# Kernel tuning notes

Hardware: AMD Instinct MI355X
Metric: run time of the kernel (lower is better)

## Reference

```python
import jax, jax.numpy as jnp
import numpy as np

N = 50000      # n_nodes
E = 300000     # n_edges
R = 32         # n_relations
D = 256        # embedding_dim
H = 128        # bilstm_hidden_size (2H == D so gate dims line up, as the source requires)
I = 64         # input_dim (time-series feature dim)
B = 4096       # batch
S = 50         # seq_len
HOPS = 2       # context_hops


def setup_inputs() -> dict:
    key = jax.random.key(0)
    ks = jax.random.split(key, 20)
    sc = 0.02
    inp = {
        "ts": jax.random.normal(ks[0], (B, S, I), jnp.float32),
        "node_emb": jax.random.normal(ks[1], (N, D), jnp.float32) * sc,
        "rel_w": jax.random.normal(ks[2], (R, D), jnp.float32) * sc + 1.0,
        "gate_W": jax.random.normal(ks[3], (D, 2 * D), jnp.float32) * sc,
        "gate_b": jnp.zeros((D,), jnp.float32),
        "risk_W1": jax.random.normal(ks[4], (D, D), jnp.float32) * sc,
        "risk_b1": jnp.zeros((D,), jnp.float32),
        "risk_W2": jax.random.normal(ks[5], (D, D), jnp.float32) * sc,
        "risk_b2": jnp.zeros((D,), jnp.float32),
        # BiLSTM encoder params (torch gate order i,f,g,o), fwd + bwd directions
        "Wih_f": jax.random.normal(ks[6], (4 * H, I), jnp.float32) * sc,
        "Whh_f": jax.random.normal(ks[7], (4 * H, H), jnp.float32) * sc,
        "b_f": jnp.zeros((4 * H,), jnp.float32),
        "Wih_b": jax.random.normal(ks[8], (4 * H, I), jnp.float32) * sc,
        "Whh_b": jax.random.normal(ks[9], (4 * H, H), jnp.float32) * sc,
        "b_b": jnp.zeros((4 * H,), jnp.float32),
        "edge_index": jax.random.randint(ks[10], (2, E), 0, N, jnp.int32),
        "edge_type": jax.random.randint(ks[11], (E,), 0, R, jnp.int32),
        "node_indexes": jax.random.randint(ks[12], (B,), 0, N, jnp.int32),
    }
    return inp


def _lstm_dir(x, Wih, Whh, b, reverse):
    # x: [B, S, I] -> outputs [B, S, H]
    def step(carry, xt):
        h, c = carry
        g = xt @ Wih.T + h @ Whh.T + b          # [B, 4H]
        i, f, gg, o = jnp.split(g, 4, axis=-1)
        c = jax.nn.sigmoid(f) * c + jax.nn.sigmoid(i) * jnp.tanh(gg)
        h = jax.nn.sigmoid(o) * jnp.tanh(c)
        return (h, c), h
    h0 = jnp.zeros((x.shape[0], Whh.shape[1]), x.dtype)
    xs = jnp.swapaxes(x, 0, 1)                   # [S, B, I]
    _, hs = jax.lax.scan(step, (h0, h0), xs, reverse=reverse)
    return jnp.swapaxes(hs, 0, 1)                # [B, S, H]


def _gcn(emb, head, tail, edge_type, rel_w, n_hops):
    # relation-weighted multi-hop message passing: gather -> relation scale -> scatter-mean
    deg = jax.ops.segment_sum(jnp.ones((head.shape[0],), emb.dtype), head, num_segments=N)
    deg = jnp.clip(deg, 1.0)[:, None]
    out = emb
    acc = emb
    for _ in range(n_hops):
        msg = out[tail] * rel_w[edge_type]                      # [E, D]
        out = jax.ops.segment_sum(msg, head, num_segments=N) / deg
        acc = acc + out
    return acc / (n_hops + 1.0)


def reference(ts, node_emb, rel_w, gate_W, gate_b, risk_W1, risk_b1, risk_W2,
              risk_b2, Wih_f, Whh_f, b_f, Wih_b, Whh_b, b_b,
              edge_index, edge_type, node_indexes):
    head, tail = edge_index[0], edge_index[1]
    all_emb = _gcn(node_emb, head, tail, edge_type, rel_w, HOPS)
    struct = all_emb[node_indexes]                              # [B, D]
    # BiLSTM encoder, temporal embedding = mean over time of [B,S,2H]
    hf = _lstm_dir(ts, Wih_f, Whh_f, b_f, reverse=False)
    hb = _lstm_dir(ts, Wih_b, Whh_b, b_b, reverse=True)
    temporal = jnp.concatenate([hf, hb], axis=-1).mean(axis=1)  # [B, 2H] == [B, D]
    cat = jnp.concatenate([struct, temporal], axis=-1)          # [B, 2D]
    gate = jax.nn.sigmoid(cat @ gate_W.T + gate_b)              # [B, D]
    merged = gate * struct + (1.0 - gate) * temporal
    risk = jnp.tanh(merged @ risk_W1.T + risk_b1) @ risk_W2.T + risk_b2
    return jax.nn.sigmoid(risk.sum(axis=-1))                    # [B]
```

## Files before the change

kernel.cpp:

```cpp
#include <hip/hip_runtime.h>

#define N_NODES 50000
#define N_EDGES 300000
#define DIM 256
#define HID 128
#define INP 64
#define BATCH 4096
#define SEQ 50
#define SCAN_BLOCKS 196

typedef float f32x2 __attribute__((ext_vector_type(2)));
typedef float f32x4 __attribute__((ext_vector_type(4)));
typedef __bf16 bf16x2 __attribute__((ext_vector_type(2)));
typedef __bf16 bf16x8 __attribute__((ext_vector_type(8)));

__device__ __forceinline__ float sigmoidf_(float x) {
    return __builtin_amdgcn_rcpf(1.0f + __expf(-x));
}
__device__ __forceinline__ float tanhf_(float x) {
    return 1.0f - 2.0f * __builtin_amdgcn_rcpf(1.0f + __expf(2.0f * x));
}

__device__ __forceinline__ void barrier_lds_only() {
    asm volatile("s_waitcnt lgkmcnt(0)" ::: "memory");
    __builtin_amdgcn_s_barrier();
}

__global__ void k_prep(const float* __restrict__ Wih_f, const float* __restrict__ Whh_f,
                       const float* __restrict__ Wih_b, const float* __restrict__ Whh_b,
                       const float* __restrict__ gate_W, const float* __restrict__ risk_W1,
                       const float* __restrict__ risk_W2, const float* __restrict__ risk_b2,
                       __bf16* __restrict__ w2frag, __bf16* __restrict__ gwp,
                       __bf16* __restrict__ w1p, float* __restrict__ w2s,
                       int* __restrict__ deg, int* __restrict__ flagi) {
    __shared__ float red[256];
    int bid = blockIdx.x, tid = threadIdx.x;
    if (bid < 768) {
        int idx = bid * 256 + tid;
        int dir = idx / 98304;
        int rem = idx % 98304;
        int frag = rem >> 9;
        int within = rem & 511;
        int lane = within >> 3, j = within & 7;
        int kc = frag % 6;
        int wg = frag / 6;
        int g = wg & 3, w = wg >> 2;
        int n = g * 128 + w * 16 + (lane & 15);
        int k = kc * 32 + (lane >> 4) * 8 + j;
        const float* Wih = dir ? Wih_b : Wih_f;
        const float* Whh = dir ? Whh_b : Whh_f;
        float v = (k < 64) ? Wih[n * 64 + k] : Whh[n * 128 + (k - 64)];
        w2frag[idx] = (__bf16)v;
    } else if (bid < 1280) {
        int idx = (bid - 768) * 256 + tid;
        int frag = idx >> 9, within = idx & 511;
        int lane = within >> 3, j = within & 7;
        int kc = frag % 16, T = frag / 16;
        int n = T * 16 + (lane & 15);
        int k = kc * 32 + (lane >> 4) * 8 + j;
        gwp[idx] = (__bf16)gate_W[(size_t)n * 512 + k];
    } else if (bid < 1536) {
        int idx = (bid - 1280) * 256 + tid;
        int frag = idx >> 9, within = idx & 511;
        int lane = within >> 3, j = within & 7;
        int kc = frag % 8, T = frag / 8;
        int n = T * 16 + (lane & 15);
        int k = kc * 32 + (lane >> 4) * 8 + j;
        w1p[idx] = (__bf16)risk_W1[(size_t)n * 256 + k];
    } else if (bid == 1536) {
        int k = tid;
        float s = 0.0f;
        for (int n = 0; n < 256; n++) s += risk_W2[(size_t)n * 256 + k];
        w2s[k] = s;
        red[k] = risk_b2[k];
        __syncthreads();
        for (int st = 128; st > 0; st >>= 1) {
            if (k < st) red[k] += red[k + st];
            __syncthreads();
        }
        if (k == 0) w2s[256] = red[0];
    } else if (bid < 1733) {
        int i = (bid - 1537) * 256 + tid;
        if (i < N_NODES) deg[i] = 0;
    } else {
        int i = (bid - 1733) * 256 + tid;
        flagi[i] = 0;
    }
}


__global__ void k_hist(const int* __restrict__ head, int* __restrict__ deg) {
    int e = blockIdx.x * 256 + threadIdx.x;
    if (e < N_EDGES) atomicAdd(&deg[head[e]], 1);
}

__global__ void k_bsum(const int* __restrict__ deg, int* __restrict__ bsum) {
    __shared__ int red[256];
    int n = blockIdx.x * 256 + threadIdx.x;
    red[threadIdx.x] = (n < N_NODES) ? deg[n] : 0;
    __syncthreads();
    for (int st = 128; st > 0; st >>= 1) {
        if (threadIdx.x < st) red[threadIdx.x] += red[threadIdx.x + st];
        __syncthreads();
    }
    if (threadIdx.x == 0) bsum[blockIdx.x] = red[0];
}

__global__ void k_scanb(const int* __restrict__ bsum, int* __restrict__ boff) {
    __shared__ int s[256];
    int i = threadIdx.x;
    int v = (i < SCAN_BLOCKS) ? bsum[i] : 0;
    s[i] = v;
    __syncthreads();
    for (int st = 1; st < 256; st <<= 1) {
        int add = (i >= st) ? s[i - st] : 0;
        __syncthreads();
        s[i] += add;
        __syncthreads();
    }
    boff[i] = s[i] - v;
}

__global__ void k_scan2(const int* __restrict__ deg, const int* __restrict__ boff,
                        int* __restrict__ offsets, int* __restrict__ cursor) {
    __shared__ int s[256];
    int i = threadIdx.x;
    int n = blockIdx.x * 256 + i;
    int v = (n < N_NODES) ? deg[n] : 0;
    s[i] = v;
    __syncthreads();
    for (int st = 1; st < 256; st <<= 1) {
        int add = (i >= st) ? s[i - st] : 0;
        __syncthreads();
        s[i] += add;
        __syncthreads();
    }
    if (n < N_NODES) {
        int off = boff[blockIdx.x] + s[i] - v;
        offsets[n] = off;
        cursor[n] = off;
    }
    if (n == 0) offsets[N_NODES] = N_EDGES;
}

__global__ void k_place(const int* __restrict__ head, const int* __restrict__ tail,
                        const int* __restrict__ etype, int* __restrict__ cursor,
                        int* __restrict__ sorted) {
    int e = blockIdx.x * 256 + threadIdx.x;
    if (e >= N_EDGES) return;
    int h = head[e];
    int pos = atomicAdd(&cursor[h], 1);
    sorted[pos] = tail[e] | (etype[e] << 16);
}

__global__ void k_flag(const int* __restrict__ nidx, const int* __restrict__ offsets,
                       const int* __restrict__ sorted, char* __restrict__ flag) {
    int b = blockIdx.x * 256 + threadIdx.x;
    if (b >= BATCH) return;
    int n = nidx[b];
    flag[n] = 1;
    int s = offsets[n], e = offsets[n + 1];
    for (int j = s; j < e; j++) flag[sorted[j] & 0xFFFF] = 1;
}

__global__ void k_gather(const int* __restrict__ offsets, const int* __restrict__ sorted,
                         const float* __restrict__ relw, const float* __restrict__ src,
                         const char* __restrict__ flag, float* __restrict__ dst) {
    int tid = threadIdx.x;
    int w = tid >> 6, lane = tid & 63;
    int n = blockIdx.x * 4 + w;
    if (n >= N_NODES) return;
    if (!flag[n]) return;
    int s = offsets[n], e = offsets[n + 1];
    f32x4 acc0 = (f32x4){0.f, 0.f, 0.f, 0.f};
    f32x4 acc1 = (f32x4){0.f, 0.f, 0.f, 0.f};
    f32x4 acc2 = (f32x4){0.f, 0.f, 0.f, 0.f};
    f32x4 acc3 = (f32x4){0.f, 0.f, 0.f, 0.f};
    int j = s;
    for (; j + 4 <= e; j += 4) {
        int p0 = sorted[j], p1 = sorted[j + 1], p2 = sorted[j + 2], p3 = sorted[j + 3];
        f32x4 v0 = *(const f32x4*)(src + (size_t)(p0 & 0xFFFF) * DIM + lane * 4);
        f32x4 v1 = *(const f32x4*)(src + (size_t)(p1 & 0xFFFF) * DIM + lane * 4);
        f32x4 v2 = *(const f32x4*)(src + (size_t)(p2 & 0xFFFF) * DIM + lane * 4);
        f32x4 v3 = *(const f32x4*)(src + (size_t)(p3 & 0xFFFF) * DIM + lane * 4);
        acc0 += v0 * *(const f32x4*)(relw + (p0 >> 16) * DIM + lane * 4);
        acc1 += v1 * *(const f32x4*)(relw + (p1 >> 16) * DIM + lane * 4);
        acc2 += v2 * *(const f32x4*)(relw + (p2 >> 16) * DIM + lane * 4);
        acc3 += v3 * *(const f32x4*)(relw + (p3 >> 16) * DIM + lane * 4);
    }
    for (; j < e; j++) {
        int p0 = sorted[j];
        f32x4 v0 = *(const f32x4*)(src + (size_t)(p0 & 0xFFFF) * DIM + lane * 4);
        acc0 += v0 * *(const f32x4*)(relw + (p0 >> 16) * DIM + lane * 4);
    }
    acc0 = (acc0 + acc1) + (acc2 + acc3);
    float inv = 1.0f / fmaxf((float)(e - s), 1.0f);
    *(f32x4*)(dst + (size_t)n * DIM + lane * 4) = acc0 * inv;
}

__global__ void k_gather2(const int* __restrict__ nidx, const int* __restrict__ offsets,
                          const int* __restrict__ sorted, const float* __restrict__ relw,
                          const float* __restrict__ out1, const float* __restrict__ emb,
                          float* __restrict__ structb) {
    int tid = threadIdx.x;
    int w = tid >> 6, lane = tid & 63;
    int b = blockIdx.x * 4 + w;
    int n = nidx[b];
    int s = offsets[n], e = offsets[n + 1];
    f32x4 acc0 = (f32x4){0.f, 0.f, 0.f, 0.f};
    f32x4 acc1 = (f32x4){0.f, 0.f, 0.f, 0.f};
    f32x4 acc2 = (f32x4){0.f, 0.f, 0.f, 0.f};
    f32x4 acc3 = (f32x4){0.f, 0.f, 0.f, 0.f};
    int j = s;
    for (; j + 4 <= e; j += 4) {
        int p0 = sorted[j], p1 = sorted[j + 1], p2 = sorted[j + 2], p3 = sorted[j + 3];
        f32x4 v0 = *(const f32x4*)(out1 + (size_t)(p0 & 0xFFFF) * DIM + lane * 4);
        f32x4 v1 = *(const f32x4*)(out1 + (size_t)(p1 & 0xFFFF) * DIM + lane * 4);
        f32x4 v2 = *(const f32x4*)(out1 + (size_t)(p2 & 0xFFFF) * DIM + lane * 4);
        f32x4 v3 = *(const f32x4*)(out1 + (size_t)(p3 & 0xFFFF) * DIM + lane * 4);
        acc0 += v0 * *(const f32x4*)(relw + (p0 >> 16) * DIM + lane * 4);
        acc1 += v1 * *(const f32x4*)(relw + (p1 >> 16) * DIM + lane * 4);
        acc2 += v2 * *(const f32x4*)(relw + (p2 >> 16) * DIM + lane * 4);
        acc3 += v3 * *(const f32x4*)(relw + (p3 >> 16) * DIM + lane * 4);
    }
    for (; j < e; j++) {
        int p0 = sorted[j];
        f32x4 v0 = *(const f32x4*)(out1 + (size_t)(p0 & 0xFFFF) * DIM + lane * 4);
        acc0 += v0 * *(const f32x4*)(relw + (p0 >> 16) * DIM + lane * 4);
    }
    acc0 = (acc0 + acc1) + (acc2 + acc3);
    float inv = 1.0f / fmaxf((float)(e - s), 1.0f);
    f32x4 o2 = acc0 * inv;
    f32x4 e0 = *(const f32x4*)(emb + (size_t)n * DIM + lane * 4);
    f32x4 o1 = *(const f32x4*)(out1 + (size_t)n * DIM + lane * 4);
    *(f32x4*)(structb + (size_t)b * DIM + lane * 4) = (e0 + o1 + o2) * (1.0f / 3.0f);
}

__launch_bounds__(512)
__global__ void k_lstm(const float* __restrict__ ts, const __bf16* __restrict__ w2frag,
                       const float* __restrict__ b_f, const float* __restrict__ b_b,
                       float* __restrict__ temporal) {
    int dir = blockIdx.y;
    int btile = blockIdx.x;
    int tid = threadIdx.x;
    int w = tid >> 6;
    int lane = tid & 63;
    int col = lane & 15, quad = lane >> 4;

    __shared__ __align__(16) __bf16 SA[2 * 16 * 200];
    __shared__ __align__(16) __bf16 SB[2 * 16 * 200];

    for (int i = tid; i < 2048; i += 512) {
        int m = i >> 7, k = i & 127;
        SA[m * 200 + 64 + k] = (__bf16)0.0f;
        SB[m * 200 + 64 + k] = (__bf16)0.0f;
    }

    const float* bias = dir ? b_b : b_f;
    float bv[4];
#pragma unroll
    for (int g = 0; g < 4; g++) bv[g] = bias[g * 128 + w * 16 + col];

    const __bf16* wbase = w2frag + (size_t)dir * 98304 + (size_t)w * 12288;
    bf16x8 wreg[24];
#pragma unroll
    for (int f = 0; f < 24; f++) {
        wreg[f] = *(const bf16x8*)(wbase + (f << 9) + lane * 8);
    }

    int sm = tid >> 5, sc = (tid & 31) * 2;
    const float* xbA = ts + ((size_t)(btile * 32 + sm) * SEQ) * INP + sc;
    const float* xbB = ts + ((size_t)(btile * 32 + 16 + sm) * SEQ) * INP + sc;
    int t0i = dir ? (SEQ - 1) : 0;
    int t1i = dir ? (SEQ - 2) : 1;
    {
        f32x2 xa = *(const f32x2*)(xbA + (size_t)t0i * INP);
        f32x2 xb = *(const f32x2*)(xbB + (size_t)t0i * INP);
        bf16x2 va; va[0] = (__bf16)xa.x; va[1] = (__bf16)xa.y;
        bf16x2 vb; vb[0] = (__bf16)xb.x; vb[1] = (__bf16)xb.y;
        *(bf16x2*)&SA[sm * 200 + sc] = va;
        *(bf16x2*)&SB[sm * 200 + sc] = vb;
    }
    f32x2 xpreA = *(const f32x2*)(xbA + (size_t)t1i * INP);
    f32x2 xpreB = *(const f32x2*)(xbB + (size_t)t1i * INP);

    f32x4 cA = (f32x4){0.f, 0.f, 0.f, 0.f}, hsA = cA;
    f32x4 cB = cA, hsB = cA;
    f32x4 accA[4], accB[4];
    int hwr = quad * 4 * 200 + 64 + w * 16 + col;
    int ard = col * 200 + quad * 8;
    barrier_lds_only();

#pragma unroll
    for (int g = 0; g < 4; g++) accA[g] = (f32x4){bv[g], bv[g], bv[g], bv[g]};
#pragma unroll
    for (int kc = 0; kc < 6; kc++) {
        bf16x8 a0 = *(const bf16x8*)&SA[ard + kc * 32];
#pragma unroll
        for (int g = 0; g < 4; g++)
            accA[g] = __builtin_amdgcn_mfma_f32_16x16x32_bf16(a0, wreg[g * 6 + kc], accA[g], 0, 0, 0);
    }

    for (int t = 0; t < SEQ; t++) {
        int cb = (t & 1) * 3200;
        int nb = ((t + 1) & 1) * 3200;

        f32x2 xnA;
        bool ldA = (t + 2 < SEQ);
        if (ldA) {
            int ti = dir ? (SEQ - 3 - t) : (t + 2);
            xnA = *(const f32x2*)(xbA + (size_t)ti * INP);
        }
#pragma unroll
        for (int g = 0; g < 4; g++) accB[g] = (f32x4){bv[g], bv[g], bv[g], bv[g]};
#pragma unroll
        for (int kc = 0; kc < 6; kc++) {
            bf16x8 a0 = *(const bf16x8*)&SB[cb + ard + kc * 32];
#pragma unroll
            for (int g = 0; g < 4; g++)
                accB[g] = __builtin_amdgcn_mfma_f32_16x16x32_bf16(a0, wreg[g * 6 + kc], accB[g], 0, 0, 0);
        }
#pragma unroll
        for (int r = 0; r < 4; r++) {
            float c = sigmoidf_(accA[1][r]) * cA[r] + sigmoidf_(accA[0][r]) * tanhf_(accA[2][r]);
            float h = sigmoidf_(accA[3][r]) * tanhf_(c);
            cA[r] = c;
            hsA[r] += h;
            SA[nb + hwr + r * 200] = (__bf16)h;
        }
        if (t + 1 < SEQ) {
            bf16x2 v; v[0] = (__bf16)xpreA.x; v[1] = (__bf16)xpreA.y;
            *(bf16x2*)&SA[nb + sm * 200 + sc] = v;
            if (ldA) xpreA = xnA;
        }
        barrier_lds_only();

        f32x2 xnB;
        bool ldB = (t + 2 < SEQ);
        if (ldB) {
            int ti = dir ? (SEQ - 3 - t) : (t + 2);
            xnB = *(const f32x2*)(xbB + (size_t)ti * INP);
        }
        if (t + 1 < SEQ) {
#pragma unroll
            for (int g = 0; g < 4; g++) accA[g] = (f32x4){bv[g], bv[g], bv[g], bv[g]};
#pragma unroll
            for (int kc = 0; kc < 6; kc++) {
                bf16x8 a0 = *(const bf16x8*)&SA[nb + ard + kc * 32];
#pragma unroll
                for (int g = 0; g < 4; g++)
                    accA[g] = __builtin_amdgcn_mfma_f32_16x16x32_bf16(a0, wreg[g * 6 + kc], accA[g], 0, 0, 0);
            }
        }
#pragma unroll
        for (int r = 0; r < 4; r++) {
            float c = sigmoidf_(accB[1][r]) * cB[r] + sigmoidf_(accB[0][r]) * tanhf_(accB[2][r]);
            float h = sigmoidf_(accB[3][r]) * tanhf_(c);
            cB[r] = c;
            hsB[r] += h;
            SB[nb + hwr + r * 200] = (__bf16)h;
        }
        if (t + 1 < SEQ) {
            bf16x2 v; v[0] = (__bf16)xpreB.x; v[1] = (__bf16)xpreB.y;
            *(bf16x2*)&SB[nb + sm * 200 + sc] = v;
            if (ldB) xpreB = xnB;
        }
        barrier_lds_only();
    }

#pragma unroll
    for (int r = 0; r < 4; r++) {
        int j = w * 16 + col;
        int bA = btile * 32 + quad * 4 + r;
        int bB = bA + 16;
        temporal[(size_t)bA * 256 + dir * 128 + j] = hsA[r] * (1.0f / SEQ);
        temporal[(size_t)bB * 256 + dir * 128 + j] = hsB[r] * (1.0f / SEQ);
    }
}


__launch_bounds__(256)
__global__ void k_head(const float* __restrict__ structb, const float* __restrict__ temporal,
                       const __bf16* __restrict__ gwp, const __bf16* __restrict__ w1p,
                       const float* __restrict__ gate_b, const float* __restrict__ risk_b1,
                       const float* __restrict__ w2s, float* __restrict__ out) {
    int bt = blockIdx.x;
    int tid = threadIdx.x;
    int w = tid >> 6, lane = tid & 63;
    int col = lane & 15, quad = lane >> 4;

    __shared__ __align__(16) __bf16 cat[16][520];
    __shared__ __align__(16) __bf16 mbuf[16][264];
    __shared__ float sacc[16];

    for (int i = tid; i < 16 * 512; i += 256) {
        int m = i >> 9, k = i & 511;
        int b = bt * 16 + m;
        float v = (k < 256) ? structb[(size_t)b * 256 + k]
                            : temporal[(size_t)b * 256 + (k - 256)];
        cat[m][k] = (__bf16)v;
    }
    if (tid < 16) sacc[tid] = 0.0f;
    __syncthreads();

    f32x4 acc[4];
#pragma unroll
    for (int ct = 0; ct < 4; ct++) {
        float b = gate_b[w * 64 + ct * 16 + col];
        acc[ct] = (f32x4){b, b, b, b};
    }
#pragma unroll
    for (int kc = 0; kc < 16; kc++) {
        bf16x8 a = *(const bf16x8*)&cat[col][kc * 32 + quad * 8];
#pragma unroll
        for (int ct = 0; ct < 4; ct++) {
            bf16x8 bf = *(const bf16x8*)(gwp + (((w * 4 + ct) * 16 + kc) << 9) + lane * 8);
            acc[ct] = __builtin_amdgcn_mfma_f32_16x16x32_bf16(a, bf, acc[ct], 0, 0, 0);
        }
    }
#pragma unroll
    for (int ct = 0; ct < 4; ct++) {
        int n = w * 64 + ct * 16 + col;
#pragma unroll
        for (int r = 0; r < 4; r++) {
            int m = quad * 4 + r;
            int b = bt * 16 + m;
            float g = sigmoidf_(acc[ct][r]);
            float s = structb[(size_t)b * 256 + n];
            float tm = temporal[(size_t)b * 256 + n];
            mbuf[m][n] = (__bf16)(g * s + (1.0f - g) * tm);
        }
    }
    __syncthreads();

    f32x4 acc2[4];
#pragma unroll
    for (int ct = 0; ct < 4; ct++) {
        float b = risk_b1[w * 64 + ct * 16 + col];
        acc2[ct] = (f32x4){b, b, b, b};
    }
#pragma unroll
    for (int kc = 0; kc < 8; kc++) {
        bf16x8 a = *(const bf16x8*)&mbuf[col][kc * 32 + quad * 8];
#pragma unroll
        for (int ct = 0; ct < 4; ct++) {
            bf16x8 bf = *(const bf16x8*)(w1p + (((w * 4 + ct) * 8 + kc) << 9) + lane * 8);
            acc2[ct] = __builtin_amdgcn_mfma_f32_16x16x32_bf16(a, bf, acc2[ct], 0, 0, 0);
        }
    }
    float part[4] = {0.f, 0.f, 0.f, 0.f};
#pragma unroll
    for (int ct = 0; ct < 4; ct++) {
        int n = w * 64 + ct * 16 + col;
        float wv = w2s[n];
#pragma unroll
        for (int r = 0; r < 4; r++) {
            part[r] += tanhf_(acc2[ct][r]) * wv;
        }
    }
#pragma unroll
    for (int off = 1; off < 16; off <<= 1) {
#pragma unroll
        for (int r = 0; r < 4; r++) part[r] += __shfl_xor(part[r], off, 64);
    }
    if (col == 0) {
#pragma unroll
        for (int r = 0; r < 4; r++) atomicAdd(&sacc[quad * 4 + r], part[r]);
    }
    __syncthreads();
    if (tid < 16) out[bt * 16 + tid] = sigmoidf_(sacc[tid] + w2s[256]);
}


extern "C" void kernel_launch(void* const* d_in, const int* in_sizes, int n_in,
                              void* d_out, int out_size, void* d_ws, size_t ws_size,
                              hipStream_t stream) {
    const float* ts       = (const float*)d_in[0];
    const float* node_emb = (const float*)d_in[1];
    const float* rel_w    = (const float*)d_in[2];
    const float* gate_W   = (const float*)d_in[3];
    const float* gate_b   = (const float*)d_in[4];
    const float* risk_W1  = (const float*)d_in[5];
    const float* risk_b1  = (const float*)d_in[6];
    const float* risk_W2  = (const float*)d_in[7];
    const float* risk_b2  = (const float*)d_in[8];
    const float* Wih_f    = (const float*)d_in[9];
    const float* Whh_f    = (const float*)d_in[10];
    const float* b_f      = (const float*)d_in[11];
    const float* Wih_b    = (const float*)d_in[12];
    const float* Whh_b    = (const float*)d_in[13];
    const float* b_b      = (const float*)d_in[14];
    const int* edge_index = (const int*)d_in[15];
    const int* edge_type  = (const int*)d_in[16];
    const int* node_idx   = (const int*)d_in[17];
    const int* head = edge_index;
    const int* tail = edge_index + N_EDGES;
    float* out = (float*)d_out;

    char* ws = (char*)d_ws;
    const size_t o_deg      = 0;
    const size_t o_flagbuf  = 200704;
    const size_t o_bsum     = o_flagbuf + 50176;
    const size_t o_boff     = o_bsum + 1024;
    const size_t o_offsets  = o_boff + 1024;
    const size_t o_cursor   = o_offsets + 200960;
    const size_t o_sorted   = o_cursor + 200704;
    const size_t o_out1     = o_sorted + 1200128;
    const size_t o_temporal = o_out1 + 51200000;
    const size_t o_struct   = o_temporal + 4194304;
    const size_t o_gwp      = o_struct + 4194304;
    const size_t o_w1p      = o_gwp + 262144;
    const size_t o_w2s      = o_w1p + 131072;
    const size_t o_w2frag   = o_w2s + 2048;

    int*    deg      = (int*)(ws + o_deg);
    char*   flag     = (char*)(ws + o_flagbuf);
    int*    flagi    = (int*)(ws + o_flagbuf);
    int*    bsum     = (int*)(ws + o_bsum);
    int*    boff     = (int*)(ws + o_boff);
    int*    offsets  = (int*)(ws + o_offsets);
    int*    cursor   = (int*)(ws + o_cursor);
    int*    sorted   = (int*)(ws + o_sorted);
    float*  out1     = (float*)(ws + o_out1);
    float*  temporal = (float*)(ws + o_temporal);
    float*  structb  = (float*)(ws + o_struct);
    __bf16* gwp      = (__bf16*)(ws + o_gwp);
    __bf16* w1p      = (__bf16*)(ws + o_w1p);
    float*  w2s      = (float*)(ws + o_w2s);
    __bf16* w2frag   = (__bf16*)(ws + o_w2frag);

    k_prep<<<1782, 256, 0, stream>>>(Wih_f, Whh_f, Wih_b, Whh_b, gate_W, risk_W1,
                                     risk_W2, risk_b2, w2frag, gwp, w1p, w2s, deg, flagi);
    k_hist<<<(N_EDGES + 255) / 256, 256, 0, stream>>>(head, deg);
    k_bsum<<<SCAN_BLOCKS, 256, 0, stream>>>(deg, bsum);
    k_scanb<<<1, 256, 0, stream>>>(bsum, boff);
    k_scan2<<<SCAN_BLOCKS, 256, 0, stream>>>(deg, boff, offsets, cursor);
    k_place<<<(N_EDGES + 255) / 256, 256, 0, stream>>>(head, tail, edge_type, cursor, sorted);
    k_flag<<<BATCH / 256, 256, 0, stream>>>(node_idx, offsets, sorted, flag);
    k_gather<<<(N_NODES + 3) / 4, 256, 0, stream>>>(offsets, sorted, rel_w, node_emb, flag, out1);
    k_lstm<<<dim3(BATCH / 32, 2), 512, 0, stream>>>(ts, w2frag, b_f, b_b, temporal);
    k_gather2<<<BATCH / 4, 256, 0, stream>>>(node_idx, offsets, sorted, rel_w, out1, node_emb, structb);
    k_head<<<BATCH / 16, 256, 0, stream>>>(structb, temporal, gwp, w1p, gate_b, risk_b1, w2s, out);
}
```

Baseline: 337.8 us.

## Split LSTM blocks to one 16-row tile each, doubling grid size

Each LSTM block used to process two 16-row batch tiles (A and B) interleaved in software, so one tile's MFMA work hid the other's gate math. Now each block handles a single 16-row tile and the grid has twice as many blocks. Launch bounds request 4 blocks per CU, so latency hiding moves from in-block interleaving to more resident waves. The risk is that each block's serial recurrence chain has less independent work per barrier, and register pressure is capped by the occupancy hint.

```diff
diff --git a/kernel.cpp b/kernel.cpp
--- a/kernel.cpp
+++ b/kernel.cpp
@@ -236,7 +236,7 @@
     *(f32x4*)(structb + (size_t)b * DIM + lane * 4) = (e0 + o1 + o2) * (1.0f / 3.0f);
 }
 
-__launch_bounds__(512)
+__launch_bounds__(512, 4)
 __global__ void k_lstm(const float* __restrict__ ts, const __bf16* __restrict__ w2frag,
                        const float* __restrict__ b_f, const float* __restrict__ b_b,
                        float* __restrict__ temporal) {
@@ -247,13 +247,11 @@
     int lane = tid & 63;
     int col = lane & 15, quad = lane >> 4;
 
-    __shared__ __align__(16) __bf16 SA[2 * 16 * 200];
-    __shared__ __align__(16) __bf16 SB[2 * 16 * 200];
+    __shared__ __align__(16) __bf16 S[2 * 16 * 200];
 
     for (int i = tid; i < 2048; i += 512) {
         int m = i >> 7, k = i & 127;
-        SA[m * 200 + 64 + k] = (__bf16)0.0f;
-        SB[m * 200 + 64 + k] = (__bf16)0.0f;
+        S[m * 200 + 64 + k] = (__bf16)0.0f;
     }
 
     const float* bias = dir ? b_b : b_f;
@@ -269,101 +267,55 @@
     }
 
     int sm = tid >> 5, sc = (tid & 31) * 2;
-    const float* xbA = ts + ((size_t)(btile * 32 + sm) * SEQ) * INP + sc;
-    const float* xbB = ts + ((size_t)(btile * 32 + 16 + sm) * SEQ) * INP + sc;
+    const float* xb = ts + ((size_t)(btile * 16 + sm) * SEQ) * INP + sc;
     int t0i = dir ? (SEQ - 1) : 0;
     int t1i = dir ? (SEQ - 2) : 1;
     {
-        f32x2 xa = *(const f32x2*)(xbA + (size_t)t0i * INP);
-        f32x2 xb = *(const f32x2*)(xbB + (size_t)t0i * INP);
+        f32x2 xa = *(const f32x2*)(xb + (size_t)t0i * INP);
         bf16x2 va; va[0] = (__bf16)xa.x; va[1] = (__bf16)xa.y;
-        bf16x2 vb; vb[0] = (__bf16)xb.x; vb[1] = (__bf16)xb.y;
-        *(bf16x2*)&SA[sm * 200 + sc] = va;
-        *(bf16x2*)&SB[sm * 200 + sc] = vb;
-    }
-    f32x2 xpreA = *(const f32x2*)(xbA + (size_t)t1i * INP);
-    f32x2 xpreB = *(const f32x2*)(xbB + (size_t)t1i * INP);
-
-    f32x4 cA = (f32x4){0.f, 0.f, 0.f, 0.f}, hsA = cA;
-    f32x4 cB = cA, hsB = cA;
-    f32x4 accA[4], accB[4];
+        *(bf16x2*)&S[sm * 200 + sc] = va;
+    }
+    f32x2 xpre = *(const f32x2*)(xb + (size_t)t1i * INP);
+
+    f32x4 c = (f32x4){0.f, 0.f, 0.f, 0.f}, hs = c;
+    f32x4 acc[4];
     int hwr = quad * 4 * 200 + 64 + w * 16 + col;
     int ard = col * 200 + quad * 8;
     barrier_lds_only();
 
-#pragma unroll
-    for (int g = 0; g < 4; g++) accA[g] = (f32x4){bv[g], bv[g], bv[g], bv[g]};
-#pragma unroll
-    for (int kc = 0; kc < 6; kc++) {
-        bf16x8 a0 = *(const bf16x8*)&SA[ard + kc * 32];
-#pragma unroll
-        for (int g = 0; g < 4; g++)
-            accA[g] = __builtin_amdgcn_mfma_f32_16x16x32_bf16(a0, wreg[g * 6 + kc], accA[g], 0, 0, 0);
-    }
-
     for (int t = 0; t < SEQ; t++) {
         int cb = (t & 1) * 3200;
         int nb = ((t + 1) & 1) * 3200;
 
-        f32x2 xnA;
-        bool ldA = (t + 2 < SEQ);
-        if (ldA) {
+        f32x2 xn;
+        bool ld = (t + 2 < SEQ);
+        if (ld) {
             int ti = dir ? (SEQ - 3 - t) : (t + 2);
-            xnA = *(const f32x2*)(xbA + (size_t)ti * INP);
-        }
-#pragma unroll
-        for (int g = 0; g < 4; g++) accB[g] = (f32x4){bv[g], bv[g], bv[g], bv[g]};
+            xn = *(const f32x2*)(xb + (size_t)ti * INP);
+        }
+
+#pragma unroll
+        for (int g = 0; g < 4; g++) acc[g] = (f32x4){bv[g], bv[g], bv[g], bv[g]};
 #pragma unroll
         for (int kc = 0; kc < 6; kc++) {
-            bf16x8 a0 = *(const bf16x8*)&SB[cb + ard + kc * 32];
+            bf16x8 a0 = *(const bf16x8*)&S[cb + ard + kc * 32];
 #pragma unroll
             for (int g = 0; g < 4; g++)
-                accB[g] = __builtin_amdgcn_mfma_f32_16x16x32_bf16(a0, wreg[g * 6 + kc], accB[g], 0, 0, 0);
-        }
+                acc[g] = __builtin_amdgcn_mfma_f32_16x16x32_bf16(a0, wreg[g * 6 + kc], acc[g], 0, 0, 0);
+        }
+
 #pragma unroll
         for (int r = 0; r < 4; r++) {
-            float c = sigmoidf_(accA[1][r]) * cA[r] + sigmoidf_(accA[0][r]) * tanhf_(accA[2][r]);
-            float h = sigmoidf_(accA[3][r]) * tanhf_(c);
-            cA[r] = c;
-            hsA[r] += h;
-            SA[nb + hwr + r * 200] = (__bf16)h;
+            float cc = sigmoidf_(acc[1][r]) * c[r] + sigmoidf_(acc[0][r]) * tanhf_(acc[2][r]);
+            float h = sigmoidf_(acc[3][r]) * tanhf_(cc);
+            c[r] = cc;
+            hs[r] += h;
+            S[nb + hwr + r * 200] = (__bf16)h;
         }
         if (t + 1 < SEQ) {
-            bf16x2 v; v[0] = (__bf16)xpreA.x; v[1] = (__bf16)xpreA.y;
-            *(bf16x2*)&SA[nb + sm * 200 + sc] = v;
-            if (ldA) xpreA = xnA;
-        }
-        barrier_lds_only();
-
-        f32x2 xnB;
-        bool ldB = (t + 2 < SEQ);
-        if (ldB) {
-            int ti = dir ? (SEQ - 3 - t) : (t + 2);
-            xnB = *(const f32x2*)(xbB + (size_t)ti * INP);
-        }
-        if (t + 1 < SEQ) {
-#pragma unroll
-            for (int g = 0; g < 4; g++) accA[g] = (f32x4){bv[g], bv[g], bv[g], bv[g]};
-#pragma unroll
-            for (int kc = 0; kc < 6; kc++) {
-                bf16x8 a0 = *(const bf16x8*)&SA[nb + ard + kc * 32];
-#pragma unroll
-                for (int g = 0; g < 4; g++)
-                    accA[g] = __builtin_amdgcn_mfma_f32_16x16x32_bf16(a0, wreg[g * 6 + kc], accA[g], 0, 0, 0);
-            }
-        }
-#pragma unroll
-        for (int r = 0; r < 4; r++) {
-            float c = sigmoidf_(accB[1][r]) * cB[r] + sigmoidf_(accB[0][r]) * tanhf_(accB[2][r]);
-            float h = sigmoidf_(accB[3][r]) * tanhf_(c);
-            cB[r] = c;
-            hsB[r] += h;
-            SB[nb + hwr + r * 200] = (__bf16)h;
-        }
-        if (t + 1 < SEQ) {
-            bf16x2 v; v[0] = (__bf16)xpreB.x; v[1] = (__bf16)xpreB.y;
-            *(bf16x2*)&SB[nb + sm * 200 + sc] = v;
-            if (ldB) xpreB = xnB;
+            bf16x2 v; v[0] = (__bf16)xpre.x; v[1] = (__bf16)xpre.y;
+            *(bf16x2*)&S[nb + sm * 200 + sc] = v;
+            if (ld) xpre = xn;
         }
         barrier_lds_only();
     }
@@ -371,10 +323,8 @@
 #pragma unroll
     for (int r = 0; r < 4; r++) {
         int j = w * 16 + col;
-        int bA = btile * 32 + quad * 4 + r;
-        int bB = bA + 16;
-        temporal[(size_t)bA * 256 + dir * 128 + j] = hsA[r] * (1.0f / SEQ);
-        temporal[(size_t)bB * 256 + dir * 128 + j] = hsB[r] * (1.0f / SEQ);
+        int b = btile * 16 + quad * 4 + r;
+        temporal[(size_t)b * 256 + dir * 128 + j] = hs[r] * (1.0f / SEQ);
     }
 }
 
@@ -538,7 +488,7 @@
     k_place<<<(N_EDGES + 255) / 256, 256, 0, stream>>>(head, tail, edge_type, cursor, sorted);
     k_flag<<<BATCH / 256, 256, 0, stream>>>(node_idx, offsets, sorted, flag);
     k_gather<<<(N_NODES + 3) / 4, 256, 0, stream>>>(offsets, sorted, rel_w, node_emb, flag, out1);
-    k_lstm<<<dim3(BATCH / 32, 2), 512, 0, stream>>>(ts, w2frag, b_f, b_b, temporal);
+    k_lstm<<<dim3(BATCH / 16, 2), 512, 0, stream>>>(ts, w2frag, b_f, b_b, temporal);
     k_gather2<<<BATCH / 4, 256, 0, stream>>>(node_idx, offsets, sorted, rel_w, out1, node_emb, structb);
     k_head<<<BATCH / 16, 256, 0, stream>>>(structb, temporal, gwp, w1p, gate_b, risk_b1, w2s, out);
 }
```

Result: slower. 488.9 us (+44.7%).
